# Kernel optimization log

Hardware: AMD Instinct MI355X
Metric: run time of the kernel (lower is better)

Reference implementation:

```python
import jax, jax.numpy as jnp
import numpy as np

N = 50000      # num_nodes
E = 400000     # num_edges
H = 64         # h_dim
R = 200        # num_rels
B = 8          # num_bases (block-diagonal decomposition)


def setup_inputs() -> dict:
    ks = jax.random.split(jax.random.key(0), 10)
    s = 1.0 / np.sqrt(H).astype(np.float32)
    return {
        "emb":     jax.random.normal(ks[0], (N, H), jnp.float32),
        "norm":    jax.random.uniform(ks[1], (E, 1), jnp.float32),
        "eps":     jax.random.normal(ks[2], (N, H), jnp.float32),
        "w1":      jax.random.normal(ks[3], (R, B * 8 * 8), jnp.float32) * s,
        "loop_w1": jax.random.normal(ks[4], (H, H), jnp.float32) * s,
        "b1":      jnp.zeros((H,), jnp.float32),
        "w2":      jax.random.normal(ks[5], (R, B * 8 * 16), jnp.float32) * s,
        "loop_w2": jax.random.normal(ks[6], (H, 2 * H), jnp.float32) * s,
        "b2":      jnp.zeros((2 * H,), jnp.float32),
        "h_ids":   jnp.arange(N, dtype=jnp.int32),
        "src":     jax.random.randint(ks[7], (E,), 0, N, jnp.int32),
        "dst":     jax.random.randint(ks[8], (E,), 0, N, jnp.int32),
        "rel":     jax.random.randint(ks[9], (E,), 0, R, jnp.int32),
    }


def bdd_conv(feat, src, dst, rel, norm, weight, loop_w, bias, out_feat):
    # RelGraphConv with 'bdd' regularizer: per-edge relation-indexed
    # block-diagonal weight gather, bmm message, norm scale, scatter-add,
    # then bias + self-loop.
    n_edges = src.shape[0]
    sub_in = feat.shape[1] // B
    sub_out = out_feat // B
    w = weight[rel].reshape(n_edges, B, sub_in, sub_out)   # gather per edge
    x = feat[src].reshape(n_edges, B, sub_in)
    msg = jnp.einsum('ebi,ebio->ebo', x, w).reshape(n_edges, out_feat) * norm
    agg = jax.ops.segment_sum(msg, dst, num_segments=feat.shape[0])
    return agg + bias + feat @ loop_w


def reference(emb, norm, eps, w1, loop_w1, b1, w2, loop_w2, b2,
              h_ids, src, dst, rel):
    feat = emb[h_ids]                                       # embedding lookup
    h1 = jax.nn.relu(bdd_conv(feat, src, dst, rel, norm, w1, loop_w1, b1, H))
    h2 = bdd_conv(h1, src, dst, rel, norm, w2, loop_w2, b2, 2 * H)
    m, raw_v = jnp.split(h2, 2, axis=-1)                    # gaussian_parameters
    v = jax.nn.softplus(raw_v) + 1e-8
    return m + jnp.sqrt(v) * eps                            # reparameterize
```

## Files before the change

### kernel.cpp

```cpp
#include <hip/hip_runtime.h>
#include <math.h>


typedef __attribute__((ext_vector_type(8))) short bf16x8;
typedef __attribute__((ext_vector_type(4))) float f32x4;
typedef __attribute__((ext_vector_type(2))) _Float16 h2;

__device__ __forceinline__ int bcasti(int v, int l) { return __builtin_amdgcn_readlane(v, l); }
__device__ __forceinline__ float bcastf(float v, int l) {
    return __int_as_float(__builtin_amdgcn_readlane(__float_as_int(v), l));
}
__device__ __forceinline__ unsigned short f2bf(float f) {
    unsigned u = __float_as_uint(f);
    return (unsigned short)((u + 0x7FFFu + ((u >> 16) & 1u)) >> 16);
}
__device__ __forceinline__ unsigned short f2h16(float f) {
    return __builtin_bit_cast(unsigned short, (_Float16)f);
}
__device__ __forceinline__ float bfs(unsigned short s) { return __uint_as_float((unsigned)s << 16); }
__device__ __forceinline__ h2 uh2(unsigned u) { return __builtin_bit_cast(h2, u); }


__global__ __launch_bounds__(256) void
blockhist(const int* __restrict__ dst, const int* __restrict__ rel,
          int* __restrict__ deg, int* __restrict__ bh, int R, int NB2, int e) {
    __shared__ int h[256];
    int t = threadIdx.x, b = blockIdx.x;
    h[t] = 0;
    __syncthreads();
    int i = b * 256 + t;
    if (i < e) {
        atomicAdd(&deg[dst[i]], 1);
        atomicAdd(&h[rel[i]], 1);
    }
    __syncthreads();
    if (t < R) bh[(size_t)t * NB2 + b] = h[t];
}

__global__ __launch_bounds__(256) void
rel_scan(int* __restrict__ bh, int* __restrict__ degr, int NB2) {
    __shared__ int sm[256];
    int r = blockIdx.x, t = threadIdx.x;
    int carry = 0;
    for (int s = 0; s < NB2; s += 256) {
        int idx = s + t;
        int v = (idx < NB2) ? bh[(size_t)r * NB2 + idx] : 0;
        sm[t] = v;
        __syncthreads();
        for (int d = 1; d < 256; d <<= 1) {
            int u = (t >= d) ? sm[t - d] : 0;
            __syncthreads();
            sm[t] += u;
            __syncthreads();
        }
        if (idx < NB2) bh[(size_t)r * NB2 + idx] = carry + sm[t] - v;
        int tot = sm[255];
        __syncthreads();
        carry += tot;
    }
    if (t == 0) degr[r] = carry;
}

__global__ void scan_part(const int* __restrict__ deg, int* __restrict__ bsum, int n) {
    __shared__ int sm[256];
    int t = threadIdx.x, g = blockIdx.x * 256 + t;
    sm[t] = (g < n) ? deg[g] : 0;
    __syncthreads();
    for (int d = 128; d > 0; d >>= 1) {
        if (t < d) sm[t] += sm[t + d];
        __syncthreads();
    }
    if (t == 0) bsum[blockIdx.x] = sm[0];
}

__global__ void scan_bsum(int* __restrict__ bsum, int* __restrict__ off, int nb, int n) {
    __shared__ int sm[256];
    int t = threadIdx.x;
    int v = (t < nb) ? bsum[t] : 0;
    sm[t] = v;
    __syncthreads();
    for (int d = 1; d < 256; d <<= 1) {
        int u = (t >= d) ? sm[t - d] : 0;
        __syncthreads();
        sm[t] += u;
        __syncthreads();
    }
    if (t < nb) bsum[t] = sm[t] - v;
    if (t == 255) off[n] = sm[255];
}

__global__ void scan_write(const int* __restrict__ deg, const int* __restrict__ bsum,
                           int* __restrict__ off, int n) {
    __shared__ int sm[256];
    int t = threadIdx.x, g = blockIdx.x * 256 + t;
    int v = (g < n) ? deg[g] : 0;
    sm[t] = v;
    __syncthreads();
    for (int d = 1; d < 256; d <<= 1) {
        int u = (t >= d) ? sm[t - d] : 0;
        __syncthreads();
        sm[t] += u;
        __syncthreads();
    }
    if (g < n) off[g] = bsum[blockIdx.x] + sm[t] - v;
}

__global__ void scan_rel(const int* __restrict__ degr, int* __restrict__ offr, int R) {
    __shared__ int sm[256];
    int t = threadIdx.x;
    int v = (t < R) ? degr[t] : 0;
    sm[t] = v;
    __syncthreads();
    for (int d = 1; d < 256; d <<= 1) {
        int u = (t >= d) ? sm[t - d] : 0;
        __syncthreads();
        sm[t] += u;
        __syncthreads();
    }
    if (t < R) offr[t] = sm[t] - v;
    if (t == 255) offr[R] = sm[255];
}

__global__ __launch_bounds__(256) void
scatter3(const int* __restrict__ src, const int* __restrict__ dst,
         const int* __restrict__ rel, const float* __restrict__ norm,
         const int* __restrict__ h_ids, const int* __restrict__ off,
         const int* __restrict__ offr, const int* __restrict__ bh,
         int* __restrict__ fil, int4* __restrict__ epk, int NB2, int e) {
    __shared__ int h[256];
    int t = threadIdx.x, b = blockIdx.x;
    h[t] = 0;
    __syncthreads();
    int i = b * 256 + t;
    if (i < e) {
        int r = rel[i], d = dst[i], s = src[i];
        int lrk = atomicAdd(&h[r], 1);
        int p = offr[r] + bh[(size_t)r * NB2 + b] + lrk;
        int q = off[d] + atomicAdd(&fil[d], 1);
        int4 v;
        v.x = h_ids[s];
        v.y = s;
        v.z = __float_as_int(norm[i]);
        v.w = q;
        epk[p] = v;
    }
}


__global__ void cvt_new(const float* __restrict__ w1, const float* __restrict__ w2,
                        const float* __restrict__ emb, unsigned short* __restrict__ w1dT,
                        unsigned short* __restrict__ w2dT, unsigned short* __restrict__ embh,
                        int R, int ne) {
    int i = blockIdx.x * blockDim.x + threadIdx.x;
    int n1d = R * 4096, n2d = R * 8192;
    if (i < n1d) {
        int r = i >> 12, rem = i & 4095;
        int c = rem >> 6, k = rem & 63;
        int b = k >> 3;
        float v = (b == (c >> 3)) ? w1[(size_t)r * 512 + b * 64 + (k & 7) * 8 + (c & 7)] : 0.f;
        w1dT[i] = f2bf(v);
    } else if (i < n1d + n2d) {
        int ii = i - n1d;
        int r = ii >> 13, rem = ii & 8191;
        int c = rem >> 6, k = rem & 63;
        int b = k >> 3;
        float v = (b == (c >> 4)) ? w2[(size_t)r * 1024 + b * 128 + (k & 7) * 16 + (c & 15)] : 0.f;
        w2dT[ii] = f2bf(v);
    } else if (i < n1d + n2d + ne) {
        int ii = i - n1d - n2d;
        embh[ii] = f2bf(emb[ii]);
    }
}

__global__ void cvt_old(const float* __restrict__ w1, const float* __restrict__ w2,
                        const float* __restrict__ emb, unsigned short* __restrict__ w1h,
                        unsigned short* __restrict__ w2h, unsigned short* __restrict__ embh,
                        int n1, int n2, int ne) {
    int i = blockIdx.x * blockDim.x + threadIdx.x;
    if (i < n1) w1h[i] = f2h16(w1[i]);
    else if (i < n1 + n2) w2h[i - n1] = f2h16(w2[i - n1]);
    else if (i < n1 + n2 + ne) embh[i - n1 - n2] = f2bf(emb[i - n1 - n2]);
}


__global__ __launch_bounds__(256) void
gemm1_mfma(const unsigned short* __restrict__ embh, const int* __restrict__ h_ids,
           const float* __restrict__ lw1, const float* __restrict__ b1,
           unsigned short* __restrict__ h1bh, int n_nodes) {
    int w = threadIdx.x >> 6, l = threadIdx.x & 63;
    int lr = l & 15, lq = l >> 4;
    int rt = blockIdx.x;
    bf16x8 bfr[2];
    int coln = w * 16 + lr;
#pragma unroll
    for (int kb = 0; kb < 2; ++kb)
#pragma unroll
        for (int jj = 0; jj < 8; ++jj)
            bfr[kb][jj] = (short)f2bf(lw1[(kb * 32 + lq * 8 + jj) * 64 + coln]);
    int nrow = rt * 16 + lr;
    if (nrow >= n_nodes) nrow = n_nodes - 1;
    const unsigned short* arow = embh + (long)h_ids[nrow] * 64 + lq * 8;
    bf16x8 af0 = *(const bf16x8*)arow;
    bf16x8 af1 = *(const bf16x8*)(arow + 32);
    f32x4 acc = {0.f, 0.f, 0.f, 0.f};
    acc = __builtin_amdgcn_mfma_f32_16x16x32_bf16(af0, bfr[0], acc, 0, 0, 0);
    acc = __builtin_amdgcn_mfma_f32_16x16x32_bf16(af1, bfr[1], acc, 0, 0, 0);
    float bb = b1[coln];
#pragma unroll
    for (int r = 0; r < 4; ++r) {
        int row = rt * 16 + lq * 4 + r;
        if (row < n_nodes) h1bh[(long)row * 64 + coln] = f2bf(acc[r] + bb);
    }
}

__global__ __launch_bounds__(256) void
gemm2_mfma(const unsigned short* __restrict__ h1h, const float* __restrict__ lw2,
           const float* __restrict__ b2, unsigned short* __restrict__ h2bh, int n_nodes) {
    int w = threadIdx.x >> 6, l = threadIdx.x & 63;
    int lr = l & 15, lq = l >> 4;
    int rt = blockIdx.x;
    bf16x8 bfr[2][2];
    int col0 = (2 * w) * 16 + lr, col1 = (2 * w + 1) * 16 + lr;
#pragma unroll
    for (int kb = 0; kb < 2; ++kb)
#pragma unroll
        for (int jj = 0; jj < 8; ++jj) {
            int k = kb * 32 + lq * 8 + jj;
            bfr[0][kb][jj] = (short)f2bf(lw2[k * 128 + col0]);
            bfr[1][kb][jj] = (short)f2bf(lw2[k * 128 + col1]);
        }
    int nrow = rt * 16 + lr;
    if (nrow >= n_nodes) nrow = n_nodes - 1;
    bf16x8 af0 = *(const bf16x8*)(h1h + (long)nrow * 64 + lq * 8);
    bf16x8 af1 = *(const bf16x8*)(h1h + (long)nrow * 64 + 32 + lq * 8);
    f32x4 acc0 = {0.f, 0.f, 0.f, 0.f}, acc1 = {0.f, 0.f, 0.f, 0.f};
    acc0 = __builtin_amdgcn_mfma_f32_16x16x32_bf16(af0, bfr[0][0], acc0, 0, 0, 0);
    acc0 = __builtin_amdgcn_mfma_f32_16x16x32_bf16(af1, bfr[0][1], acc0, 0, 0, 0);
    acc1 = __builtin_amdgcn_mfma_f32_16x16x32_bf16(af0, bfr[1][0], acc1, 0, 0, 0);
    acc1 = __builtin_amdgcn_mfma_f32_16x16x32_bf16(af1, bfr[1][1], acc1, 0, 0, 0);
    float bb0 = b2[col0], bb1 = b2[col1];
#pragma unroll
    for (int r = 0; r < 4; ++r) {
        int row = rt * 16 + lq * 4 + r;
        if (row < n_nodes) {
            h2bh[(long)row * 128 + col0] = f2bf(acc0[r] + bb0);
            h2bh[(long)row * 128 + col1] = f2bf(acc1[r] + bb1);
        }
    }
}


__global__ __launch_bounds__(256) void
gemm_rel1(const unsigned short* __restrict__ embh, const unsigned short* __restrict__ w1dT,
          const int4* __restrict__ epk, const int* __restrict__ offr,
          _Float16* __restrict__ msg1, int S) {
    int r = blockIdx.x / S, s = blockIdx.x % S;
    int w = threadIdx.x >> 6, l = threadIdx.x & 63;
    int lr = l & 15, lq = l >> 4;
    int e0r = offr[r], e1r = offr[r + 1];
    if (e0r >= e1r) return;
    bf16x8 bfr[4][2];
    const unsigned short* wb = w1dT + (size_t)r * 4096;
#pragma unroll
    for (int ct = 0; ct < 4; ++ct)
#pragma unroll
        for (int kb = 0; kb < 2; ++kb)
            bfr[ct][kb] = *(const bf16x8*)(wb + (ct * 16 + lr) * 64 + kb * 32 + lq * 8);
    for (int t = s * 4 + w;; t += S * 4) {
        int t16 = e0r + t * 16;
        if (t16 >= e1r) break;
        int erow = t16 + lr;
        int erc = erow < e1r ? erow : e1r - 1;
        int xa = epk[erc].x;
        const unsigned short* arow = embh + (size_t)xa * 64 + lq * 8;
        bf16x8 af0 = *(const bf16x8*)arow;
        bf16x8 af1 = *(const bf16x8*)(arow + 32);
        f32x4 acc[4];
#pragma unroll
        for (int ct = 0; ct < 4; ++ct) {
            acc[ct] = (f32x4){0.f, 0.f, 0.f, 0.f};
            acc[ct] = __builtin_amdgcn_mfma_f32_16x16x32_bf16(af0, bfr[ct][0], acc[ct], 0, 0, 0);
            acc[ct] = __builtin_amdgcn_mfma_f32_16x16x32_bf16(af1, bfr[ct][1], acc[ct], 0, 0, 0);
        }
#pragma unroll
        for (int r4 = 0; r4 < 4; ++r4) {
            int orow = t16 + lq * 4 + r4;
            int orc = orow < e1r ? orow : e1r - 1;
            int2 nq = *(const int2*)(&epk[orc].z);
            float nm = __int_as_float(nq.x);
            size_t q = (size_t)nq.y;
            if (orow < e1r) {
#pragma unroll
                for (int ct = 0; ct < 4; ++ct)
                    msg1[q * 64 + ct * 16 + lr] = (_Float16)(acc[ct][r4] * nm);
            }
        }
    }
}

__global__ __launch_bounds__(256) void
gemm_rel2(const unsigned short* __restrict__ h1h, const unsigned short* __restrict__ w2dT,
          const int4* __restrict__ epk, const int* __restrict__ offr,
          _Float16* __restrict__ msg2, int S) {
    int r = blockIdx.x / S, s = blockIdx.x % S;
    int w = threadIdx.x >> 6, l = threadIdx.x & 63;
    int lr = l & 15, lq = l >> 4;
    int e0r = offr[r], e1r = offr[r + 1];
    if (e0r >= e1r) return;
    bf16x8 bfr[8][2];
    const unsigned short* wb = w2dT + (size_t)r * 8192;
#pragma unroll
    for (int ct = 0; ct < 8; ++ct)
#pragma unroll
        for (int kb = 0; kb < 2; ++kb)
            bfr[ct][kb] = *(const bf16x8*)(wb + (ct * 16 + lr) * 64 + kb * 32 + lq * 8);
    for (int t = s * 4 + w;; t += S * 4) {
        int t16 = e0r + t * 16;
        if (t16 >= e1r) break;
        int erow = t16 + lr;
        int erc = erow < e1r ? erow : e1r - 1;
        int xb = epk[erc].y;
        const unsigned short* arow = h1h + (size_t)xb * 64 + lq * 8;
        bf16x8 af0 = *(const bf16x8*)arow;
        bf16x8 af1 = *(const bf16x8*)(arow + 32);
        f32x4 acc[8];
#pragma unroll
        for (int ct = 0; ct < 8; ++ct) {
            acc[ct] = (f32x4){0.f, 0.f, 0.f, 0.f};
            acc[ct] = __builtin_amdgcn_mfma_f32_16x16x32_bf16(af0, bfr[ct][0], acc[ct], 0, 0, 0);
            acc[ct] = __builtin_amdgcn_mfma_f32_16x16x32_bf16(af1, bfr[ct][1], acc[ct], 0, 0, 0);
        }
#pragma unroll
        for (int r4 = 0; r4 < 4; ++r4) {
            int orow = t16 + lq * 4 + r4;
            int orc = orow < e1r ? orow : e1r - 1;
            int2 nq = *(const int2*)(&epk[orc].z);
            float nm = __int_as_float(nq.x);
            size_t q = (size_t)nq.y;
            if (orow < e1r) {
#pragma unroll
                for (int ct = 0; ct < 8; ++ct)
                    msg2[q * 128 + ct * 16 + lr] = (_Float16)(acc[ct][r4] * nm);
            }
        }
    }
}


__global__ __launch_bounds__(256) void
sum1(const _Float16* __restrict__ msg1, const unsigned short* __restrict__ h1bh,
     const int* __restrict__ off, unsigned short* __restrict__ h1h, int n_nodes) {
    int tid = threadIdx.x;
    int w = tid >> 6, j = tid & 63;
    int n = blockIdx.x * 4 + w;
    if (n >= n_nodes) return;
    float base = bfs(h1bh[(size_t)n * 64 + j]);
    int e0 = off[n], e1v = off[n + 1];
    float a0 = 0.f, a1 = 0.f, a2 = 0.f, a3 = 0.f;
    int r = e0;
    for (; r + 4 <= e1v; r += 4) {
        a0 += (float)msg1[(size_t)(r + 0) * 64 + j];
        a1 += (float)msg1[(size_t)(r + 1) * 64 + j];
        a2 += (float)msg1[(size_t)(r + 2) * 64 + j];
        a3 += (float)msg1[(size_t)(r + 3) * 64 + j];
    }
    for (; r < e1v; ++r) a0 += (float)msg1[(size_t)r * 64 + j];
    h1h[(size_t)n * 64 + j] = f2bf(fmaxf(a0 + a1 + a2 + a3 + base, 0.f));
}

__global__ __launch_bounds__(256) void
sum2(const _Float16* __restrict__ msg2, const unsigned short* __restrict__ h2bh,
     const float* __restrict__ eps, const int* __restrict__ off,
     float* __restrict__ out, int n_nodes) {
    int tid = threadIdx.x;
    int w = tid >> 6, j = tid & 63;
    int n = blockIdx.x * 4 + w;
    if (n >= n_nodes) return;
    float basem = bfs(h2bh[(size_t)n * 128 + j]);
    float basev = bfs(h2bh[(size_t)n * 128 + 64 + j]);
    int e0 = off[n], e1v = off[n + 1];
    float m0 = 0.f, m1 = 0.f, v0 = 0.f, v1a = 0.f;
    int r = e0;
    for (; r + 2 <= e1v; r += 2) {
        m0  += (float)msg2[(size_t)(r + 0) * 128 + j];
        v0  += (float)msg2[(size_t)(r + 0) * 128 + 64 + j];
        m1  += (float)msg2[(size_t)(r + 1) * 128 + j];
        v1a += (float)msg2[(size_t)(r + 1) * 128 + 64 + j];
    }
    for (; r < e1v; ++r) {
        m0 += (float)msg2[(size_t)r * 128 + j];
        v0 += (float)msg2[(size_t)r * 128 + 64 + j];
    }
    float vm = m0 + m1 + basem;
    float vv = v0 + v1a + basev;
    float sp = (vv > 20.f) ? vv : log1pf(expf(vv));
    out[(size_t)n * 64 + j] = fmaf(sqrtf(sp + 1e-8f), eps[(size_t)n * 64 + j], vm);
}


__global__ void hist2(const int* __restrict__ dst, const int* __restrict__ rel,
                      int* __restrict__ deg, int* __restrict__ degr, int e) {
    int i = blockIdx.x * blockDim.x + threadIdx.x;
    if (i < e) {
        atomicAdd(&deg[dst[i]], 1);
        atomicAdd(&degr[rel[i]], 1);
    }
}

__global__ void scatter_pack(const int* __restrict__ src, const int* __restrict__ dst,
                             const int* __restrict__ rel, const float* __restrict__ norm,
                             const int* __restrict__ h_ids, const int* __restrict__ off,
                             int* __restrict__ fil, unsigned* __restrict__ packA,
                             unsigned* __restrict__ packB, float* __restrict__ norm_s, int e) {
    int i = blockIdx.x * blockDim.x + threadIdx.x;
    if (i >= e) return;
    int d = dst[i];
    int p = off[d] + atomicAdd(&fil[d], 1);
    unsigned rhi = (unsigned)rel[i] << 16;
    int s = src[i];
    packA[p] = (unsigned)h_ids[s] | rhi;
    packB[p] = (unsigned)s | rhi;
    norm_s[p] = norm[i];
}

__device__ __forceinline__ float reduce8(float a0, float a1, float a2, float a3,
                                         float a4, float a5, float a6, float a7, int i) {
    int p1 = i & 1, p2 = (i >> 1) & 1, p3 = (i >> 2) & 1;
    float ka, sb, u0, u1, u2, u3, w0, w1;
    ka = p1 ? a1 : a0; sb = p1 ? a0 : a1; u0 = ka + __shfl_xor(sb, 1, 64);
    ka = p1 ? a3 : a2; sb = p1 ? a2 : a3; u1 = ka + __shfl_xor(sb, 1, 64);
    ka = p1 ? a5 : a4; sb = p1 ? a4 : a5; u2 = ka + __shfl_xor(sb, 1, 64);
    ka = p1 ? a7 : a6; sb = p1 ? a6 : a7; u3 = ka + __shfl_xor(sb, 1, 64);
    ka = p2 ? u1 : u0; sb = p2 ? u0 : u1; w0 = ka + __shfl_xor(sb, 2, 64);
    ka = p2 ? u3 : u2; sb = p2 ? u2 : u3; w1 = ka + __shfl_xor(sb, 2, 64);
    ka = p3 ? w1 : w0; sb = p3 ? w0 : w1;
    return ka + __shfl_xor(sb, 4, 64);
}

__global__ __launch_bounds__(256) void
edge1(const unsigned short* __restrict__ embh, const unsigned short* __restrict__ w1h,
      const unsigned short* __restrict__ h1bh, const int* __restrict__ off,
      const unsigned* __restrict__ packA, const float* __restrict__ norm_s,
      unsigned short* __restrict__ h1h, int n_nodes) {
    __shared__ unsigned short xstage[4][8][64];
    int tid = threadIdx.x;
    int w = tid >> 6, j = tid & 63, i = j & 7;
    int cl = j >> 3, il = j & 7;
    int n = blockIdx.x * 4 + w;
    if (n >= n_nodes) return;
    unsigned short* xsw = &xstage[w][0][0];
    float base = bfs(h1bh[(long)n * 64 + j]);
    h2 acc[4];
#pragma unroll
    for (int q = 0; q < 4; ++q) acc[q] = (h2){(_Float16)0.f, (_Float16)0.f};
    int e0 = off[n], e1v = off[n + 1];
    const long woff = (long)j * 8;
    for (int win = e0; win < e1v; win += 64) {
        int wcnt = e1v - win; if (wcnt > 64) wcnt = 64;
        unsigned u = (j < wcnt) ? packA[win + j] : 0u;
        float nmv = (j < wcnt) ? norm_s[win + j] : 0.f;
        for (int b8 = 0; b8 < wcnt; b8 += 8) {
            int cnt = wcnt - b8; if (cnt > 8) cnt = 8;
            int uc = __builtin_amdgcn_ds_bpermute((b8 + cl) << 2, (int)u);
            if (cl < cnt)
                *(bf16x8*)(xsw + (cl << 6) + (il << 3)) =
                    *(const bf16x8*)(embh + (long)((unsigned)uc & 0xFFFFu) * 64 + (il << 3));
            asm volatile("s_waitcnt lgkmcnt(0)" ::: "memory");
#pragma unroll
            for (int c = 0; c < 8; ++c)
                if (c < cnt) {
                    float nm = bcastf(nmv, b8 + c);
                    int rr = bcasti((int)u, b8 + c) >> 16;
                    uint4 wd = *(const uint4*)(w1h + (long)rr * 512 + woff);
                    _Float16 xh = (_Float16)(bfs(xsw[(c << 6) + j]) * nm);
                    h2 xh2 = {xh, xh};
                    acc[0] += xh2 * uh2(wd.x);
                    acc[1] += xh2 * uh2(wd.y);
                    acc[2] += xh2 * uh2(wd.z);
                    acc[3] += xh2 * uh2(wd.w);
                }
        }
    }
    float agg = reduce8((float)acc[0].x, (float)acc[0].y, (float)acc[1].x, (float)acc[1].y,
                        (float)acc[2].x, (float)acc[2].y, (float)acc[3].x, (float)acc[3].y, i);
    h1h[(long)n * 64 + j] = f2bf(fmaxf(base + agg, 0.f));
}

__global__ __launch_bounds__(256) void
edge2(const unsigned short* __restrict__ h1h, const unsigned short* __restrict__ w2h,
      const unsigned short* __restrict__ h2bh, const float* __restrict__ eps,
      const int* __restrict__ off, const unsigned* __restrict__ packB,
      const float* __restrict__ norm_s, float* __restrict__ out, int n_nodes) {
    __shared__ unsigned short xstage[4][8][64];
    int tid = threadIdx.x;
    int w = tid >> 6, j = tid & 63;
    int i = j & 7, b = j >> 3;
    int o1 = b * 16 + i, o2 = o1 + 8;
    int cl = j >> 3, il = j & 7;
    int n = blockIdx.x * 4 + w;
    if (n >= n_nodes) return;
    unsigned short* xsw = &xstage[w][0][0];
    float base1 = bfs(h2bh[(long)n * 128 + o1]);
    float base2 = bfs(h2bh[(long)n * 128 + o2]);
    h2 acc[8];
#pragma unroll
    for (int q = 0; q < 8; ++q) acc[q] = (h2){(_Float16)0.f, (_Float16)0.f};
    int e0 = off[n], e1v = off[n + 1];
    const long woff = (long)j * 16;
    for (int win = e0; win < e1v; win += 64) {
        int wcnt = e1v - win; if (wcnt > 64) wcnt = 64;
        unsigned u = (j < wcnt) ? packB[win + j] : 0u;
        float nmv = (j < wcnt) ? norm_s[win + j] : 0.f;
        for (int b8 = 0; b8 < wcnt; b8 += 8) {
            int cnt = wcnt - b8; if (cnt > 8) cnt = 8;
            int uc = __builtin_amdgcn_ds_bpermute((b8 + cl) << 2, (int)u);
            if (cl < cnt)
                *(bf16x8*)(xsw + (cl << 6) + (il << 3)) =
                    *(const bf16x8*)(h1h + (long)((unsigned)uc & 0xFFFFu) * 64 + (il << 3));
            asm volatile("s_waitcnt lgkmcnt(0)" ::: "memory");
#pragma unroll
            for (int c = 0; c < 8; ++c)
                if (c < cnt) {
                    float nm = bcastf(nmv, b8 + c);
                    int rr = bcasti((int)u, b8 + c) >> 16;
                    const uint4* p = (const uint4*)(w2h + (long)rr * 1024 + woff);
                    uint4 wa = p[0], wb = p[1];
                    _Float16 xh = (_Float16)(bfs(xsw[(c << 6) + j]) * nm);
                    h2 xh2 = {xh, xh};
                    acc[0] += xh2 * uh2(wa.x);
                    acc[1] += xh2 * uh2(wa.y);
                    acc[2] += xh2 * uh2(wa.z);
                    acc[3] += xh2 * uh2(wa.w);
                    acc[4] += xh2 * uh2(wb.x);
                    acc[5] += xh2 * uh2(wb.y);
                    acc[6] += xh2 * uh2(wb.z);
                    acc[7] += xh2 * uh2(wb.w);
                }
        }
    }
    float r1 = reduce8((float)acc[0].x, (float)acc[0].y, (float)acc[1].x, (float)acc[1].y,
                       (float)acc[2].x, (float)acc[2].y, (float)acc[3].x, (float)acc[3].y, i);
    float r2 = reduce8((float)acc[4].x, (float)acc[4].y, (float)acc[5].x, (float)acc[5].y,
                       (float)acc[6].x, (float)acc[6].y, (float)acc[7].x, (float)acc[7].y, i);
    float v1 = r1 + base1;
    float v2 = r2 + base2;
    float p1 = __shfl_xor(v1, 32, 64);
    float p2 = __shfl_xor(v2, 32, 64);
    if (j < 32) {
        long basep = (long)n * 64;
        float sp1 = (p1 > 20.f) ? p1 : log1pf(expf(p1));
        float sp2 = (p2 > 20.f) ? p2 : log1pf(expf(p2));
        out[basep + o1] = fmaf(sqrtf(sp1 + 1e-8f), eps[basep + o1], v1);
        out[basep + o2] = fmaf(sqrtf(sp2 + 1e-8f), eps[basep + o2], v2);
    }
}


extern "C" void kernel_launch(void* const* d_in, const int* in_sizes, int n_in,
                              void* d_out, int out_size, void* d_ws, size_t ws_size,
                              hipStream_t stream) {
    const float* emb   = (const float*)d_in[0];
    const float* norm  = (const float*)d_in[1];
    const float* eps   = (const float*)d_in[2];
    const float* w1    = (const float*)d_in[3];
    const float* lw1   = (const float*)d_in[4];
    const float* b1    = (const float*)d_in[5];
    const float* w2    = (const float*)d_in[6];
    const float* lw2   = (const float*)d_in[7];
    const float* b2    = (const float*)d_in[8];
    const int*   h_ids = (const int*)d_in[9];
    const int*   src   = (const int*)d_in[10];
    const int*   dst   = (const int*)d_in[11];
    const int*   rel   = (const int*)d_in[12];
    float* out = (float*)d_out;

    int n_nodes = in_sizes[0] / 64;
    int n_edges = in_sizes[10];
    int nw1 = in_sizes[3];
    int nw2 = in_sizes[6];
    int ne  = in_sizes[0];
    int R   = nw1 / 512;

    int blk = 256;
    int nb = (n_nodes + 255) / 256;
    int nt = (n_nodes + 15) / 16;
    int ng = (n_nodes + 3) / 4;
    int NB2 = (n_edges + 255) / 256;

    size_t need = (size_t)ne * 2
                + (size_t)n_nodes * 64 * 2 * 2
                + (size_t)n_nodes * 128 * 2
                + (size_t)R * 4096 * 2
                + (size_t)R * 8192 * 2
                + (size_t)n_edges * 16
                + (size_t)n_edges * 128 * 2
                + (size_t)(2 * n_nodes + R) * 4
                + (size_t)R * NB2 * 4
                + (size_t)(n_nodes + 1) * 4
                + (size_t)(R + 1) * 4
                + (size_t)nb * 4;

    if (ws_size >= need && R <= 256) {
        char* p = (char*)d_ws;
        unsigned short* embh = (unsigned short*)p;  p += (size_t)ne * 2;
        unsigned short* h1bh = (unsigned short*)p;  p += (size_t)n_nodes * 64 * 2;
        unsigned short* h1h  = (unsigned short*)p;  p += (size_t)n_nodes * 64 * 2;
        unsigned short* h2bh = (unsigned short*)p;  p += (size_t)n_nodes * 128 * 2;
        unsigned short* w1dT = (unsigned short*)p;  p += (size_t)R * 4096 * 2;
        unsigned short* w2dT = (unsigned short*)p;  p += (size_t)R * 8192 * 2;
        int4*  epk = (int4*)p;                      p += (size_t)n_edges * 16;
        _Float16* msg = (_Float16*)p;               p += (size_t)n_edges * 128 * 2;
        int* deg  = (int*)p;                        p += (size_t)n_nodes * 4;
        int* fil  = (int*)p;                        p += (size_t)n_nodes * 4;
        int* degr = (int*)p;                        p += (size_t)R * 4;
        int* bh   = (int*)p;                        p += (size_t)R * NB2 * 4;
        int* off  = (int*)p;                        p += (size_t)(n_nodes + 1) * 4;
        int* offr = (int*)p;                        p += (size_t)(R + 1) * 4;
        int* bsum = (int*)p;

        const int S = 16;
        int ncv = R * 4096 + R * 8192 + ne;
        hipMemsetAsync(deg, 0, (size_t)(2 * n_nodes) * 4, stream);
        cvt_new<<<(ncv + blk - 1) / blk, blk, 0, stream>>>(w1, w2, emb, w1dT, w2dT, embh, R, ne);
        blockhist<<<NB2, blk, 0, stream>>>(dst, rel, deg, bh, R, NB2, n_edges);
        scan_part<<<nb, 256, 0, stream>>>(deg, bsum, n_nodes);
        scan_bsum<<<1, 256, 0, stream>>>(bsum, off, nb, n_nodes);
        scan_write<<<nb, 256, 0, stream>>>(deg, bsum, off, n_nodes);
        rel_scan<<<R, 256, 0, stream>>>(bh, degr, NB2);
        scan_rel<<<1, 256, 0, stream>>>(degr, offr, R);
        scatter3<<<NB2, blk, 0, stream>>>(src, dst, rel, norm, h_ids, off, offr, bh,
                                          fil, epk, NB2, n_edges);
        gemm1_mfma<<<nt, blk, 0, stream>>>(embh, h_ids, lw1, b1, h1bh, n_nodes);
        gemm_rel1<<<R * S, blk, 0, stream>>>(embh, w1dT, epk, offr, msg, S);
        sum1<<<ng, blk, 0, stream>>>(msg, h1bh, off, h1h, n_nodes);
        gemm2_mfma<<<nt, blk, 0, stream>>>(h1h, lw2, b2, h2bh, n_nodes);
        gemm_rel2<<<R * S, blk, 0, stream>>>(h1h, w2dT, epk, offr, msg, S);
        sum2<<<ng, blk, 0, stream>>>(msg, h2bh, eps, off, out, n_nodes);
    } else {
        char* p = (char*)d_ws;
        unsigned short* h1bh = (unsigned short*)p;  p += (size_t)n_nodes * 64 * 2;
        unsigned short* h1h  = (unsigned short*)p;  p += (size_t)n_nodes * 64 * 2;
        unsigned short* h2bh = (unsigned short*)p;  p += (size_t)n_nodes * 128 * 2;
        unsigned short* embh = (unsigned short*)p;  p += (size_t)ne * 2;
        unsigned short* w1h  = (unsigned short*)p;  p += (size_t)nw1 * 2;
        unsigned short* w2h  = (unsigned short*)p;  p += (size_t)nw2 * 2;
        unsigned* pkA = (unsigned*)p;               p += (size_t)n_edges * 4;
        unsigned* pkB = (unsigned*)p;               p += (size_t)n_edges * 4;
        float* norm_s = (float*)p;                  p += (size_t)n_edges * 4;
        int* deg  = (int*)p;                        p += (size_t)n_nodes * 4;
        int* fil  = (int*)p;                        p += (size_t)n_nodes * 4;
        int* degr = (int*)p;                        p += (size_t)R * 4;
        int* filr = (int*)p;                        p += (size_t)R * 4;
        int* off  = (int*)p;                        p += (size_t)(n_nodes + 1) * 4;
        int* bsum = (int*)p;

        hipMemsetAsync(deg, 0, (size_t)(2 * n_nodes + 2 * R) * 4, stream);
        cvt_old<<<(nw1 + nw2 + ne + blk - 1) / blk, blk, 0, stream>>>(w1, w2, emb, w1h, w2h, embh, nw1, nw2, ne);
        hist2<<<(n_edges + blk - 1) / blk, blk, 0, stream>>>(dst, rel, deg, degr, n_edges);
        scan_part<<<nb, 256, 0, stream>>>(deg, bsum, n_nodes);
        scan_bsum<<<1, 256, 0, stream>>>(bsum, off, nb, n_nodes);
        scan_write<<<nb, 256, 0, stream>>>(deg, bsum, off, n_nodes);
        scatter_pack<<<(n_edges + blk - 1) / blk, blk, 0, stream>>>(
            src, dst, rel, norm, h_ids, off, fil, pkA, pkB, norm_s, n_edges);
        gemm1_mfma<<<nt, blk, 0, stream>>>(embh, h_ids, lw1, b1, h1bh, n_nodes);
        edge1<<<ng, blk, 0, stream>>>(embh, w1h, h1bh, off, pkA, norm_s, h1h, n_nodes);
        gemm2_mfma<<<nt, blk, 0, stream>>>(h1h, lw2, b2, h2bh, n_nodes);
        edge2<<<ng, blk, 0, stream>>>(h1h, w2h, h2bh, eps, off, pkB, norm_s, out, n_nodes);
    }
}
```

Before: 318.6 us.

## Replace dst-CSR message buffer and segment sums with fp32 atomic scatter-add

Drops the destination-degree histogram, three-pass node scan, and per-edge fp16 message buffer. The relation-grouped GEMM kernels now atomically add scaled messages straight into fp32 node accumulators that the self-loop GEMMs have already initialised. Simple elementwise epilogues then apply ReLU/bf16 conversion and the softplus reparameterisation. This removes several kernels and the large message write and read, at the cost of many fp32 global atomics and non-deterministic summation order.

After: 423.6 us. 33.0% more time.

```diff
diff --git a/kernel.cpp b/kernel.cpp
--- a/kernel.cpp
+++ b/kernel.cpp
@@ -22,17 +22,13 @@
 
 
 __global__ __launch_bounds__(256) void
-blockhist(const int* __restrict__ dst, const int* __restrict__ rel,
-          int* __restrict__ deg, int* __restrict__ bh, int R, int NB2, int e) {
+relhist(const int* __restrict__ rel, int* __restrict__ bh, int R, int NB2, int e) {
     __shared__ int h[256];
     int t = threadIdx.x, b = blockIdx.x;
     h[t] = 0;
     __syncthreads();
     int i = b * 256 + t;
-    if (i < e) {
-        atomicAdd(&deg[dst[i]], 1);
-        atomicAdd(&h[rel[i]], 1);
-    }
+    if (i < e) atomicAdd(&h[rel[i]], 1);
     __syncthreads();
     if (t < R) bh[(size_t)t * NB2 + b] = h[t];
 }
@@ -61,50 +57,6 @@
     if (t == 0) degr[r] = carry;
 }
 
-__global__ void scan_part(const int* __restrict__ deg, int* __restrict__ bsum, int n) {
-    __shared__ int sm[256];
-    int t = threadIdx.x, g = blockIdx.x * 256 + t;
-    sm[t] = (g < n) ? deg[g] : 0;
-    __syncthreads();
-    for (int d = 128; d > 0; d >>= 1) {
-        if (t < d) sm[t] += sm[t + d];
-        __syncthreads();
-    }
-    if (t == 0) bsum[blockIdx.x] = sm[0];
-}
-
-__global__ void scan_bsum(int* __restrict__ bsum, int* __restrict__ off, int nb, int n) {
-    __shared__ int sm[256];
-    int t = threadIdx.x;
-    int v = (t < nb) ? bsum[t] : 0;
-    sm[t] = v;
-    __syncthreads();
-    for (int d = 1; d < 256; d <<= 1) {
-        int u = (t >= d) ? sm[t - d] : 0;
-        __syncthreads();
-        sm[t] += u;
-        __syncthreads();
-    }
-    if (t < nb) bsum[t] = sm[t] - v;
-    if (t == 255) off[n] = sm[255];
-}
-
-__global__ void scan_write(const int* __restrict__ deg, const int* __restrict__ bsum,
-                           int* __restrict__ off, int n) {
-    __shared__ int sm[256];
-    int t = threadIdx.x, g = blockIdx.x * 256 + t;
-    int v = (g < n) ? deg[g] : 0;
-    sm[t] = v;
-    __syncthreads();
-    for (int d = 1; d < 256; d <<= 1) {
-        int u = (t >= d) ? sm[t - d] : 0;
-        __syncthreads();
-        sm[t] += u;
-        __syncthreads();
-    }
-    if (g < n) off[g] = bsum[blockIdx.x] + sm[t] - v;
-}
-
 __global__ void scan_rel(const int* __restrict__ degr, int* __restrict__ offr, int R) {
     __shared__ int sm[256];
     int t = threadIdx.x;
@@ -122,26 +74,24 @@
 }
 
 __global__ __launch_bounds__(256) void
-scatter3(const int* __restrict__ src, const int* __restrict__ dst,
+scatterR(const int* __restrict__ src, const int* __restrict__ dst,
          const int* __restrict__ rel, const float* __restrict__ norm,
-         const int* __restrict__ h_ids, const int* __restrict__ off,
-         const int* __restrict__ offr, const int* __restrict__ bh,
-         int* __restrict__ fil, int4* __restrict__ epk, int NB2, int e) {
+         const int* __restrict__ h_ids, const int* __restrict__ offr,
+         const int* __restrict__ bh, int4* __restrict__ epk, int NB2, int e) {
     __shared__ int h[256];
     int t = threadIdx.x, b = blockIdx.x;
     h[t] = 0;
     __syncthreads();
     int i = b * 256 + t;
     if (i < e) {
-        int r = rel[i], d = dst[i], s = src[i];
+        int r = rel[i], s = src[i];
         int lrk = atomicAdd(&h[r], 1);
         int p = offr[r] + bh[(size_t)r * NB2 + b] + lrk;
-        int q = off[d] + atomicAdd(&fil[d], 1);
         int4 v;
         v.x = h_ids[s];
         v.y = s;
         v.z = __float_as_int(norm[i]);
-        v.w = q;
+        v.w = dst[i];
         epk[p] = v;
     }
 }
@@ -184,9 +134,9 @@
 
 
 __global__ __launch_bounds__(256) void
-gemm1_mfma(const unsigned short* __restrict__ embh, const int* __restrict__ h_ids,
-           const float* __restrict__ lw1, const float* __restrict__ b1,
-           unsigned short* __restrict__ h1bh, int n_nodes) {
+gemm1f(const unsigned short* __restrict__ embh, const int* __restrict__ h_ids,
+       const float* __restrict__ lw1, const float* __restrict__ b1,
+       float* __restrict__ h1acc, int n_nodes) {
     int w = threadIdx.x >> 6, l = threadIdx.x & 63;
     int lr = l & 15, lq = l >> 4;
     int rt = blockIdx.x;
@@ -209,13 +159,13 @@
 #pragma unroll
     for (int r = 0; r < 4; ++r) {
         int row = rt * 16 + lq * 4 + r;
-        if (row < n_nodes) h1bh[(long)row * 64 + coln] = f2bf(acc[r] + bb);
-    }
-}
-
-__global__ __launch_bounds__(256) void
-gemm2_mfma(const unsigned short* __restrict__ h1h, const float* __restrict__ lw2,
-           const float* __restrict__ b2, unsigned short* __restrict__ h2bh, int n_nodes) {
+        if (row < n_nodes) h1acc[(long)row * 64 + coln] = acc[r] + bb;
+    }
+}
+
+__global__ __launch_bounds__(256) void
+gemm2f(const unsigned short* __restrict__ h1h, const float* __restrict__ lw2,
+       const float* __restrict__ b2, float* __restrict__ h2acc, int n_nodes) {
     int w = threadIdx.x >> 6, l = threadIdx.x & 63;
     int lr = l & 15, lq = l >> 4;
     int rt = blockIdx.x;
@@ -243,8 +193,8 @@
     for (int r = 0; r < 4; ++r) {
         int row = rt * 16 + lq * 4 + r;
         if (row < n_nodes) {
-            h2bh[(long)row * 128 + col0] = f2bf(acc0[r] + bb0);
-            h2bh[(long)row * 128 + col1] = f2bf(acc1[r] + bb1);
+            h2acc[(long)row * 128 + col0] = acc0[r] + bb0;
+            h2acc[(long)row * 128 + col1] = acc1[r] + bb1;
         }
     }
 }
@@ -253,7 +203,7 @@
 __global__ __launch_bounds__(256) void
 gemm_rel1(const unsigned short* __restrict__ embh, const unsigned short* __restrict__ w1dT,
           const int4* __restrict__ epk, const int* __restrict__ offr,
-          _Float16* __restrict__ msg1, int S) {
+          float* __restrict__ h1acc, int S) {
     int r = blockIdx.x / S, s = blockIdx.x % S;
     int w = threadIdx.x >> 6, l = threadIdx.x & 63;
     int lr = l & 15, lq = l >> 4;
@@ -285,14 +235,13 @@
 #pragma unroll
         for (int r4 = 0; r4 < 4; ++r4) {
             int orow = t16 + lq * 4 + r4;
-            int orc = orow < e1r ? orow : e1r - 1;
-            int2 nq = *(const int2*)(&epk[orc].z);
-            float nm = __int_as_float(nq.x);
-            size_t q = (size_t)nq.y;
             if (orow < e1r) {
+                int2 nq = *(const int2*)(&epk[orow].z);
+                float nm = __int_as_float(nq.x);
+                size_t dn = (size_t)nq.y;
 #pragma unroll
                 for (int ct = 0; ct < 4; ++ct)
-                    msg1[q * 64 + ct * 16 + lr] = (_Float16)(acc[ct][r4] * nm);
+                    atomicAdd(&h1acc[dn * 64 + ct * 16 + lr], acc[ct][r4] * nm);
             }
         }
     }
@@ -301,7 +250,7 @@
 __global__ __launch_bounds__(256) void
 gemm_rel2(const unsigned short* __restrict__ h1h, const unsigned short* __restrict__ w2dT,
           const int4* __restrict__ epk, const int* __restrict__ offr,
-          _Float16* __restrict__ msg2, int S) {
+          float* __restrict__ h2acc, int S) {
     int r = blockIdx.x / S, s = blockIdx.x % S;
     int w = threadIdx.x >> 6, l = threadIdx.x & 63;
     int lr = l & 15, lq = l >> 4;
@@ -333,14 +282,13 @@
 #pragma unroll
         for (int r4 = 0; r4 < 4; ++r4) {
             int orow = t16 + lq * 4 + r4;
-            int orc = orow < e1r ? orow : e1r - 1;
-            int2 nq = *(const int2*)(&epk[orc].z);
-            float nm = __int_as_float(nq.x);
-            size_t q = (size_t)nq.y;
             if (orow < e1r) {
+                int2 nq = *(const int2*)(&epk[orow].z);
+                float nm = __int_as_float(nq.x);
+                size_t dn = (size_t)nq.y;
 #pragma unroll
                 for (int ct = 0; ct < 8; ++ct)
-                    msg2[q * 128 + ct * 16 + lr] = (_Float16)(acc[ct][r4] * nm);
+                    atomicAdd(&h2acc[dn * 128 + ct * 16 + lr], acc[ct][r4] * nm);
             }
         }
     }
@@ -348,53 +296,21 @@
 
 
 __global__ __launch_bounds__(256) void
-sum1(const _Float16* __restrict__ msg1, const unsigned short* __restrict__ h1bh,
-     const int* __restrict__ off, unsigned short* __restrict__ h1h, int n_nodes) {
-    int tid = threadIdx.x;
-    int w = tid >> 6, j = tid & 63;
-    int n = blockIdx.x * 4 + w;
-    if (n >= n_nodes) return;
-    float base = bfs(h1bh[(size_t)n * 64 + j]);
-    int e0 = off[n], e1v = off[n + 1];
-    float a0 = 0.f, a1 = 0.f, a2 = 0.f, a3 = 0.f;
-    int r = e0;
-    for (; r + 4 <= e1v; r += 4) {
-        a0 += (float)msg1[(size_t)(r + 0) * 64 + j];
-        a1 += (float)msg1[(size_t)(r + 1) * 64 + j];
-        a2 += (float)msg1[(size_t)(r + 2) * 64 + j];
-        a3 += (float)msg1[(size_t)(r + 3) * 64 + j];
-    }
-    for (; r < e1v; ++r) a0 += (float)msg1[(size_t)r * 64 + j];
-    h1h[(size_t)n * 64 + j] = f2bf(fmaxf(a0 + a1 + a2 + a3 + base, 0.f));
-}
-
-__global__ __launch_bounds__(256) void
-sum2(const _Float16* __restrict__ msg2, const unsigned short* __restrict__ h2bh,
-     const float* __restrict__ eps, const int* __restrict__ off,
-     float* __restrict__ out, int n_nodes) {
-    int tid = threadIdx.x;
-    int w = tid >> 6, j = tid & 63;
-    int n = blockIdx.x * 4 + w;
-    if (n >= n_nodes) return;
-    float basem = bfs(h2bh[(size_t)n * 128 + j]);
-    float basev = bfs(h2bh[(size_t)n * 128 + 64 + j]);
-    int e0 = off[n], e1v = off[n + 1];
-    float m0 = 0.f, m1 = 0.f, v0 = 0.f, v1a = 0.f;
-    int r = e0;
-    for (; r + 2 <= e1v; r += 2) {
-        m0  += (float)msg2[(size_t)(r + 0) * 128 + j];
-        v0  += (float)msg2[(size_t)(r + 0) * 128 + 64 + j];
-        m1  += (float)msg2[(size_t)(r + 1) * 128 + j];
-        v1a += (float)msg2[(size_t)(r + 1) * 128 + 64 + j];
-    }
-    for (; r < e1v; ++r) {
-        m0 += (float)msg2[(size_t)r * 128 + j];
-        v0 += (float)msg2[(size_t)r * 128 + 64 + j];
-    }
-    float vm = m0 + m1 + basem;
-    float vv = v0 + v1a + basev;
+ep1(const float* __restrict__ h1acc, unsigned short* __restrict__ h1h, int total) {
+    int i = blockIdx.x * blockDim.x + threadIdx.x;
+    if (i < total) h1h[i] = f2bf(fmaxf(h1acc[i], 0.f));
+}
+
+__global__ __launch_bounds__(256) void
+ep2(const float* __restrict__ h2acc, const float* __restrict__ eps,
+    float* __restrict__ out, int total) {
+    int i = blockIdx.x * blockDim.x + threadIdx.x;
+    if (i >= total) return;
+    int n = i >> 6, j = i & 63;
+    float vm = h2acc[(size_t)n * 128 + j];
+    float vv = h2acc[(size_t)n * 128 + 64 + j];
     float sp = (vv > 20.f) ? vv : log1pf(expf(vv));
-    out[(size_t)n * 64 + j] = fmaf(sqrtf(sp + 1e-8f), eps[(size_t)n * 64 + j], vm);
+    out[i] = fmaf(sqrtf(sp + 1e-8f), eps[i], vm);
 }
 
 
@@ -405,6 +321,50 @@
         atomicAdd(&deg[dst[i]], 1);
         atomicAdd(&degr[rel[i]], 1);
     }
+}
+
+__global__ void scan_part(const int* __restrict__ deg, int* __restrict__ bsum, int n) {
+    __shared__ int sm[256];
+    int t = threadIdx.x, g = blockIdx.x * 256 + t;
+    sm[t] = (g < n) ? deg[g] : 0;
+    __syncthreads();
+    for (int d = 128; d > 0; d >>= 1) {
+        if (t < d) sm[t] += sm[t + d];
+        __syncthreads();
+    }
+    if (t == 0) bsum[blockIdx.x] = sm[0];
+}
+
+__global__ void scan_bsum(int* __restrict__ bsum, int* __restrict__ off, int nb, int n) {
+    __shared__ int sm[256];
+    int t = threadIdx.x;
+    int v = (t < nb) ? bsum[t] : 0;
+    sm[t] = v;
+    __syncthreads();
+    for (int d = 1; d < 256; d <<= 1) {
+        int u = (t >= d) ? sm[t - d] : 0;
+        __syncthreads();
+        sm[t] += u;
+        __syncthreads();
+    }
+    if (t < nb) bsum[t] = sm[t] - v;
+    if (t == 255) off[n] = sm[255];
+}
+
+__global__ void scan_write(const int* __restrict__ deg, const int* __restrict__ bsum,
+                           int* __restrict__ off, int n) {
+    __shared__ int sm[256];
+    int t = threadIdx.x, g = blockIdx.x * 256 + t;
+    int v = (g < n) ? deg[g] : 0;
+    sm[t] = v;
+    __syncthreads();
+    for (int d = 1; d < 256; d <<= 1) {
+        int u = (t >= d) ? sm[t - d] : 0;
+        __syncthreads();
+        sm[t] += u;
+        __syncthreads();
+    }
+    if (g < n) off[g] = bsum[blockIdx.x] + sm[t] - v;
 }
 
 __global__ void scatter_pack(const int* __restrict__ src, const int* __restrict__ dst,
@@ -435,6 +395,72 @@
     ka = p2 ? u3 : u2; sb = p2 ? u2 : u3; w1 = ka + __shfl_xor(sb, 2, 64);
     ka = p3 ? w1 : w0; sb = p3 ? w0 : w1;
     return ka + __shfl_xor(sb, 4, 64);
+}
+
+__global__ __launch_bounds__(256) void
+gemm1_mfma(const unsigned short* __restrict__ embh, const int* __restrict__ h_ids,
+           const float* __restrict__ lw1, const float* __restrict__ b1,
+           unsigned short* __restrict__ h1bh, int n_nodes) {
+    int w = threadIdx.x >> 6, l = threadIdx.x & 63;
+    int lr = l & 15, lq = l >> 4;
+    int rt = blockIdx.x;
+    bf16x8 bfr[2];
+    int coln = w * 16 + lr;
+#pragma unroll
+    for (int kb = 0; kb < 2; ++kb)
+#pragma unroll
+        for (int jj = 0; jj < 8; ++jj)
+            bfr[kb][jj] = (short)f2bf(lw1[(kb * 32 + lq * 8 + jj) * 64 + coln]);
+    int nrow = rt * 16 + lr;
+    if (nrow >= n_nodes) nrow = n_nodes - 1;
+    const unsigned short* arow = embh + (long)h_ids[nrow] * 64 + lq * 8;
+    bf16x8 af0 = *(const bf16x8*)arow;
+    bf16x8 af1 = *(const bf16x8*)(arow + 32);
+    f32x4 acc = {0.f, 0.f, 0.f, 0.f};
+    acc = __builtin_amdgcn_mfma_f32_16x16x32_bf16(af0, bfr[0], acc, 0, 0, 0);
+    acc = __builtin_amdgcn_mfma_f32_16x16x32_bf16(af1, bfr[1], acc, 0, 0, 0);
+    float bb = b1[coln];
+#pragma unroll
+    for (int r = 0; r < 4; ++r) {
+        int row = rt * 16 + lq * 4 + r;
+        if (row < n_nodes) h1bh[(long)row * 64 + coln] = f2bf(acc[r] + bb);
+    }
+}
+
+__global__ __launch_bounds__(256) void
+gemm2_mfma(const unsigned short* __restrict__ h1h, const float* __restrict__ lw2,
+           const float* __restrict__ b2, unsigned short* __restrict__ h2bh, int n_nodes) {
+    int w = threadIdx.x >> 6, l = threadIdx.x & 63;
+    int lr = l & 15, lq = l >> 4;
+    int rt = blockIdx.x;
+    bf16x8 bfr[2][2];
+    int col0 = (2 * w) * 16 + lr, col1 = (2 * w + 1) * 16 + lr;
+#pragma unroll
+    for (int kb = 0; kb < 2; ++kb)
+#pragma unroll
+        for (int jj = 0; jj < 8; ++jj) {
+            int k = kb * 32 + lq * 8 + jj;
+            bfr[0][kb][jj] = (short)f2bf(lw2[k * 128 + col0]);
+            bfr[1][kb][jj] = (short)f2bf(lw2[k * 128 + col1]);
+        }
+    int nrow = rt * 16 + lr;
+    if (nrow >= n_nodes) nrow = n_nodes - 1;
+    bf16x8 af0 = *(const bf16x8*)(h1h + (long)nrow * 64 + lq * 8);
+    bf16x8 af1 = *(const bf16x8*)(h1h + (long)nrow * 64 + 32 + lq * 8);
+    f32x4 acc0 = {0.f, 0.f, 0.f, 0.f}, acc1 = {0.f, 0.f, 0.f, 0.f};
+    acc0 = __builtin_amdgcn_mfma_f32_16x16x32_bf16(af0, bfr[0][0], acc0, 0, 0, 0);
+    acc0 = __builtin_amdgcn_mfma_f32_16x16x32_bf16(af1, bfr[0][1], acc0, 0, 0, 0);
+    acc1 = __builtin_amdgcn_mfma_f32_16x16x32_bf16(af0, bfr[1][0], acc1, 0, 0, 0);
+    acc1 = __builtin_amdgcn_mfma_f32_16x16x32_bf16(af1, bfr[1][1], acc1, 0, 0, 0);
+    float bb0 = b2[col0], bb1 = b2[col1];
+#pragma unroll
+    for (int r = 0; r < 4; ++r) {
+        int row = rt * 16 + lq * 4 + r;
+        if (row < n_nodes) {
+            h2bh[(long)row * 128 + col0] = f2bf(acc0[r] + bb0);
+            h2bh[(long)row * 128 + col1] = f2bf(acc1[r] + bb1);
+        }
+    }
 }
 
 __global__ __launch_bounds__(256) void
@@ -584,59 +610,47 @@
     int blk = 256;
     int nb = (n_nodes + 255) / 256;
     int nt = (n_nodes + 15) / 16;
-    int ng = (n_nodes + 3) / 4;
     int NB2 = (n_edges + 255) / 256;
 
     size_t need = (size_t)ne * 2
-                + (size_t)n_nodes * 64 * 2 * 2
-                + (size_t)n_nodes * 128 * 2
                 + (size_t)R * 4096 * 2
                 + (size_t)R * 8192 * 2
                 + (size_t)n_edges * 16
-                + (size_t)n_edges * 128 * 2
-                + (size_t)(2 * n_nodes + R) * 4
+                + (size_t)n_nodes * 64 * 4
+                + (size_t)n_nodes * 128 * 4
+                + (size_t)n_nodes * 64 * 2
                 + (size_t)R * NB2 * 4
-                + (size_t)(n_nodes + 1) * 4
-                + (size_t)(R + 1) * 4
-                + (size_t)nb * 4;
+                + (size_t)R * 4
+                + (size_t)(R + 1) * 4;
 
     if (ws_size >= need && R <= 256) {
         char* p = (char*)d_ws;
         unsigned short* embh = (unsigned short*)p;  p += (size_t)ne * 2;
-        unsigned short* h1bh = (unsigned short*)p;  p += (size_t)n_nodes * 64 * 2;
-        unsigned short* h1h  = (unsigned short*)p;  p += (size_t)n_nodes * 64 * 2;
-        unsigned short* h2bh = (unsigned short*)p;  p += (size_t)n_nodes * 128 * 2;
         unsigned short* w1dT = (unsigned short*)p;  p += (size_t)R * 4096 * 2;
         unsigned short* w2dT = (unsigned short*)p;  p += (size_t)R * 8192 * 2;
         int4*  epk = (int4*)p;                      p += (size_t)n_edges * 16;
-        _Float16* msg = (_Float16*)p;               p += (size_t)n_edges * 128 * 2;
-        int* deg  = (int*)p;                        p += (size_t)n_nodes * 4;
-        int* fil  = (int*)p;                        p += (size_t)n_nodes * 4;
+        float* h1acc = (float*)p;                   p += (size_t)n_nodes * 64 * 4;
+        float* h2acc = (float*)p;                   p += (size_t)n_nodes * 128 * 4;
+        unsigned short* h1h = (unsigned short*)p;   p += (size_t)n_nodes * 64 * 2;
+        int* bh   = (int*)p;                        p += (size_t)R * NB2 * 4;
         int* degr = (int*)p;                        p += (size_t)R * 4;
-        int* bh   = (int*)p;                        p += (size_t)R * NB2 * 4;
-        int* off  = (int*)p;                        p += (size_t)(n_nodes + 1) * 4;
-        int* offr = (int*)p;                        p += (size_t)(R + 1) * 4;
-        int* bsum = (int*)p;
+        int* offr = (int*)p;
 
         const int S = 16;
         int ncv = R * 4096 + R * 8192 + ne;
-        hipMemsetAsync(deg, 0, (size_t)(2 * n_nodes) * 4, stream);
         cvt_new<<<(ncv + blk - 1) / blk, blk, 0, stream>>>(w1, w2, emb, w1dT, w2dT, embh, R, ne);
-        blockhist<<<NB2, blk, 0, stream>>>(dst, rel, deg, bh, R, NB2, n_edges);
-        scan_part<<<nb, 256, 0, stream>>>(deg, bsum, n_nodes);
-        scan_bsum<<<1, 256, 0, stream>>>(bsum, off, nb, n_nodes);
-        scan_write<<<nb, 256, 0, stream>>>(deg, bsum, off, n_nodes);
+        relhist<<<NB2, blk, 0, stream>>>(rel, bh, R, NB2, n_edges);
         rel_scan<<<R, 256, 0, stream>>>(bh, degr, NB2);
         scan_rel<<<1, 256, 0, stream>>>(degr, offr, R);
-        scatter3<<<NB2, blk, 0, stream>>>(src, dst, rel, norm, h_ids, off, offr, bh,
-                                          fil, epk, NB2, n_edges);
-        gemm1_mfma<<<nt, blk, 0, stream>>>(embh, h_ids, lw1, b1, h1bh, n_nodes);
-        gemm_rel1<<<R * S, blk, 0, stream>>>(embh, w1dT, epk, offr, msg, S);
-        sum1<<<ng, blk, 0, stream>>>(msg, h1bh, off, h1h, n_nodes);
-        gemm2_mfma<<<nt, blk, 0, stream>>>(h1h, lw2, b2, h2bh, n_nodes);
-        gemm_rel2<<<R * S, blk, 0, stream>>>(h1h, w2dT, epk, offr, msg, S);
-        sum2<<<ng, blk, 0, stream>>>(msg, h2bh, eps, off, out, n_nodes);
+        scatterR<<<NB2, blk, 0, stream>>>(src, dst, rel, norm, h_ids, offr, bh, epk, NB2, n_edges);
+        gemm1f<<<nt, blk, 0, stream>>>(embh, h_ids, lw1, b1, h1acc, n_nodes);
+        gemm_rel1<<<R * S, blk, 0, stream>>>(embh, w1dT, epk, offr, h1acc, S);
+        ep1<<<(n_nodes * 64 + blk - 1) / blk, blk, 0, stream>>>(h1acc, h1h, n_nodes * 64);
+        gemm2f<<<nt, blk, 0, stream>>>(h1h, lw2, b2, h2acc, n_nodes);
+        gemm_rel2<<<R * S, blk, 0, stream>>>(h1h, w2dT, epk, offr, h2acc, S);
+        ep2<<<(n_nodes * 64 + blk - 1) / blk, blk, 0, stream>>>(h2acc, eps, out, n_nodes * 64);
     } else {
+        int ng = (n_nodes + 3) / 4;
         char* p = (char*)d_ws;
         unsigned short* h1bh = (unsigned short*)p;  p += (size_t)n_nodes * 64 * 2;
         unsigned short* h1h  = (unsigned short*)p;  p += (size_t)n_nodes * 64 * 2;
```
